# Performance work log

Measured on AMD Instinct MI355X. Metric: run time of the kernel, lower is better.

## Reference

```python
import jax, jax.numpy as jnp
import numpy as np

D_MODEL = 768
N_HEAD = 12
D_K = D_MODEL // N_HEAD  # 64, also d_v
B, S = 2, 2048


def setup_inputs() -> dict:
    key = jax.random.key(0)
    ks = jax.random.split(key, 8)
    scale = 1.0 / np.sqrt(D_MODEL)
    return {
        "q": jax.random.normal(ks[0], (B, S, D_MODEL), dtype=jnp.float32),
        "k": jax.random.normal(ks[1], (B, S, D_MODEL), dtype=jnp.float32),
        "v": jax.random.normal(ks[2], (B, S, D_MODEL), dtype=jnp.float32),
        "mask": jax.random.randint(ks[3], (B, 1, S, S), 0, 2, dtype=jnp.int32),
        # per-head projection weights, stacked over heads: [H, d_model, d_k]
        "Wq": jax.random.normal(ks[4], (N_HEAD, D_MODEL, D_K), dtype=jnp.float32) * scale,
        "Wk": jax.random.normal(ks[5], (N_HEAD, D_MODEL, D_K), dtype=jnp.float32) * scale,
        "Wv": jax.random.normal(ks[6], (N_HEAD, D_MODEL, D_K), dtype=jnp.float32) * scale,
        # output projection: [n_head*d_v, d_model]
        "Wo": jax.random.normal(ks[7], (N_HEAD * D_K, D_MODEL), dtype=jnp.float32) * scale,
    }


def reference(q, k, v, mask, Wq, Wk, Wv, Wo):
    # Per-head projections (batched over heads instead of a python loop)
    qh = jnp.einsum("bsd,hdk->bhsk", q, Wq)  # [B,H,S,d_k]
    kh = jnp.einsum("bsd,hdk->bhsk", k, Wk)
    vh = jnp.einsum("bsd,hdk->bhsk", v, Wv)
    # Scaled dot-product attention with full score matrix (faithful to source)
    scores = jnp.einsum("bhsk,bhtk->bhst", qh, kh) / jnp.sqrt(jnp.asarray(D_K, qh.dtype))
    scores = jnp.where(mask == 0, jnp.asarray(-1e9, scores.dtype), scores)
    attn = jax.nn.softmax(scores, axis=-1)  # [B,H,S,S]
    out = jnp.einsum("bhst,bhtk->bhsk", attn, vh)  # [B,H,S,d_k]
    # concat heads (matches torch.cat over head outputs along last dim)
    out = out.transpose(0, 2, 1, 3).reshape(out.shape[0], out.shape[2], -1)  # [B,S,H*d_k]
    return out @ Wo  # [B,S,d_model]
```

## Files before the change

kernel.cpp:

```cpp
#include <hip/hip_runtime.h>
#include <stdint.h>

#define S_LEN 2048
#define NH 12
#define DM 768
#define DK 64
#define NB 2
#define MROWS (NB * S_LEN)

typedef __attribute__((ext_vector_type(8))) short short8;
typedef __attribute__((ext_vector_type(4))) float f32x4;
typedef __attribute__((ext_vector_type(4))) uint32_t u32x4;

__device__ __forceinline__ unsigned short bf16rne(float f) {
    union { float f; uint32_t u; } v; v.f = f;
    return (unsigned short)((v.u + 0x7FFFu + ((v.u >> 16) & 1u)) >> 16);
}

__device__ __forceinline__ uint32_t cvtpk(float lo, float hi) {
    uint32_t r;
    asm("v_cvt_pk_bf16_f32 %0, %1, %2" : "=v"(r) : "v"(lo), "v"(hi));
    return r;
}

__global__ __launch_bounds__(256) void prep_kernel(
        const float* __restrict__ Wq, const float* __restrict__ Wk,
        const float* __restrict__ Wv, const float* __restrict__ Wo,
        const int* __restrict__ mask,
        unsigned short* __restrict__ WqT, unsigned short* __restrict__ WkT,
        unsigned short* __restrict__ WvT, unsigned short* __restrict__ WoT,
        uint32_t* __restrict__ pm) {
    int bx = blockIdx.x;
    if (bx < 9216) {
        int which = bx / 2304;
        const float* W = (which == 0) ? Wq : (which == 1) ? Wk : (which == 2) ? Wv : Wo;
        unsigned short* WT = (which == 0) ? WqT : (which == 1) ? WkT : (which == 2) ? WvT : WoT;
        int idx = (bx % 2304) * 256 + threadIdx.x;
        int n = idx / DM, kd = idx % DM;
        float val;
        if (which < 3) { int h = n >> 6, kk = n & 63; val = W[(h * DM + kd) * DK + kk]; }
        else          { val = W[kd * DM + n]; }
        if (which == 0) val *= 0.18033688011112042f;
        WT[idx] = bf16rne(val);
    } else {
        int t = (bx - 9216) * 256 + threadIdx.x;
        const int4* mp = (const int4*)mask;
        int4 a = mp[2 * t], b = mp[2 * t + 1];
        unsigned int by =
            (a.x != 0 ? 1u : 0u)  | (a.y != 0 ? 2u : 0u)  | (a.z != 0 ? 4u : 0u)  | (a.w != 0 ? 8u : 0u) |
            (b.x != 0 ? 16u : 0u) | (b.y != 0 ? 32u : 0u) | (b.z != 0 ? 64u : 0u) | (b.w != 0 ? 128u : 0u);
        ((unsigned char*)pm)[t] = (unsigned char)by;
    }
}

__device__ __forceinline__ void gemm_core_f32A(const float* __restrict__ A,
                                               const unsigned short* __restrict__ BT,
                                               unsigned short* As, unsigned short* Bs,
                                               f32x4 (&acc)[4][4]) {
    const int tid = threadIdx.x;
    const int lane = tid & 63, wid = tid >> 6;
    const int ww = wid & 1, wh = wid >> 1;
    const int quad = lane >> 4, l16 = lane & 15;
    const int lr = lane >> 2;
    const int lc = (lane & 3) * 8;
    typedef __attribute__((address_space(1))) const unsigned int* gp1;
    typedef __attribute__((address_space(3))) unsigned int* lp3;
    const float* Ag0 = A + (size_t)(wid * 32 + lr) * DM + lc;
    const float* Ag1 = A + (size_t)(wid * 32 + 16 + lr) * DM + lc;
    const unsigned short* Bg = BT + (size_t)(wid * 32 + lr) * DM + lc;
    unsigned short* Al = &As[wid * 32 * 32];
    unsigned short* Bl = &Bs[wid * 32 * 32];
    for (int kt = 0; kt < DM; kt += 32) {
        __syncthreads();
        __builtin_amdgcn_global_load_lds((gp1)(const void*)(Bg + kt),            (lp3)(void*)Bl,             16, 0, 0);
        __builtin_amdgcn_global_load_lds((gp1)(const void*)(Bg + 16 * DM + kt),  (lp3)(void*)(Bl + 16 * 32), 16, 0, 0);
        float4 x0 = *(const float4*)(Ag0 + kt), x1 = *(const float4*)(Ag0 + kt + 4);
        float4 y0 = *(const float4*)(Ag1 + kt), y1 = *(const float4*)(Ag1 + kt + 4);
        u32x4 ua, ub;
        ua[0] = cvtpk(x0.x, x0.y); ua[1] = cvtpk(x0.z, x0.w);
        ua[2] = cvtpk(x1.x, x1.y); ua[3] = cvtpk(x1.z, x1.w);
        ub[0] = cvtpk(y0.x, y0.y); ub[1] = cvtpk(y0.z, y0.w);
        ub[2] = cvtpk(y1.x, y1.y); ub[3] = cvtpk(y1.z, y1.w);
        *(u32x4*)&Al[lr * 32 + lc] = ua;
        *(u32x4*)&Al[(16 + lr) * 32 + lc] = ub;
        __syncthreads();
        short8 af[4], bf[4];
#pragma unroll
        for (int i = 0; i < 4; ++i) af[i] = *(const short8*)&As[(wh * 64 + i * 16 + l16) * 32 + quad * 8];
#pragma unroll
        for (int j = 0; j < 4; ++j) bf[j] = *(const short8*)&Bs[(ww * 64 + j * 16 + l16) * 32 + quad * 8];
#pragma unroll
        for (int i = 0; i < 4; ++i)
#pragma unroll
            for (int j = 0; j < 4; ++j)
                acc[i][j] = __builtin_amdgcn_mfma_f32_16x16x32_bf16(af[i], bf[j], acc[i][j], 0, 0, 0);
    }
}

__global__ __launch_bounds__(256) void proj_gemm(
        const float* __restrict__ qf32, const float* __restrict__ kf32,
        const float* __restrict__ vf32,
        const unsigned short* __restrict__ WqT, const unsigned short* __restrict__ WkT,
        const unsigned short* __restrict__ WvT,
        unsigned short* __restrict__ qh, unsigned short* __restrict__ kh,
        unsigned short* __restrict__ vhT) {
    __shared__ __align__(16) unsigned short As[128 * 32];
    __shared__ __align__(16) unsigned short Bs[128 * 32];
    const int z = blockIdx.z;
    const float* A = (z == 0) ? qf32 : (z == 1) ? kf32 : vf32;
    const unsigned short* BT = (z == 0) ? WqT : (z == 1) ? WkT : WvT;
    f32x4 acc[4][4] = {};
    gemm_core_f32A(A + (size_t)blockIdx.x * 128 * DM, BT + (size_t)blockIdx.y * 128 * DM, As, Bs, acc);

    const int tid = threadIdx.x;
    const int lane = tid & 63, wid = tid >> 6;
    const int ww = wid & 1, wh = wid >> 1;
    const int quad = lane >> 4, l16 = lane & 15;
    const int row0 = blockIdx.x * 128 + wh * 64;
    const int col0 = blockIdx.y * 128 + ww * 64;
    if (z < 2) {
        unsigned short* C = z ? kh : qh;
#pragma unroll
        for (int i = 0; i < 4; ++i)
#pragma unroll
            for (int j = 0; j < 4; ++j)
#pragma unroll
                for (int r = 0; r < 4; ++r)
                    C[(size_t)(row0 + i * 16 + quad * 4 + r) * DM + col0 + j * 16 + l16] = bf16rne(acc[i][j][r]);
    } else {
#pragma unroll
        for (int i = 0; i < 4; ++i)
#pragma unroll
            for (int j = 0; j < 4; ++j) {
                int row = row0 + i * 16 + quad * 4;
                int col = col0 + j * 16 + l16;
                int bb = row >> 11, s = row & 2047;
                int hh = col >> 6, d = col & 63;
                int g = (s >> 2) & 15;
                int pg = (g & 8) | ((g & 3) << 1) | ((g & 4) >> 2);
                int sp = (s & ~63) | (pg << 2) | (s & 3);
                uint32_t lo = (uint32_t)bf16rne(acc[i][j][0]) | ((uint32_t)bf16rne(acc[i][j][1]) << 16);
                uint32_t hi = (uint32_t)bf16rne(acc[i][j][2]) | ((uint32_t)bf16rne(acc[i][j][3]) << 16);
                uint2 o = make_uint2(lo, hi);
                *(uint2*)&vhT[(size_t)((bb * NH + hh) * DK + d) * S_LEN + sp] = o;
            }
    }
}

__global__ __launch_bounds__(256) void attn_kernel(
        const unsigned short* __restrict__ qh, const unsigned short* __restrict__ kh,
        const unsigned short* __restrict__ vhT, const uint32_t* __restrict__ pm,
        unsigned short* __restrict__ pob, float* __restrict__ lsb) {
    const int bid = blockIdx.x;
    const int xcd = bid & 7, pos = bid >> 3;
    const int wkr = xcd * 192 + pos;
    const int qt = wkr & 15;
    const int hz = wkr >> 4;
    const int h = hz % 12;
    const int z = hz / 12;
    const int b = z >> 2, ks = z & 3;
    const int tid = threadIdx.x, w = tid >> 6, lane = tid & 63;
    const int quad = lane >> 4, l16 = lane & 15;
    __shared__ __align__(16) unsigned short SMEM[2 * 64 * 64];
    unsigned short* Ks = SMEM;
    unsigned short* Vs = SMEM + 64 * 64;

    const int qrow0 = qt * 128 + w * 32;
    short8 qf[2][2];
#pragma unroll
    for (int mi = 0; mi < 2; ++mi) {
        const size_t qbase = (size_t)(b * S_LEN + qrow0 + mi * 16 + l16) * DM + h * DK;
        qf[mi][0] = *(const short8*)&qh[qbase + quad * 8];
        qf[mi][1] = *(const short8*)&qh[qbase + 32 + quad * 8];
    }
    short8 of = {};
    if (l16 == 0) {
#pragma unroll
        for (int j = 0; j < 8; ++j) of[j] = (short)0x3F80;
    }

    f32x4 out_t[2][4] = {};
    f32x4 outl[2] = {};

    const int srow = tid >> 2, scol = (tid & 3) << 4;
    const int ssw = (srow & 7) << 3;
    const int sc0 = srow * 64 + (scol ^ ssw);
    const int sc1 = srow * 64 + ((scol + 8) ^ ssw);
    const unsigned short* Kg = kh + (size_t)b * S_LEN * DM + h * DK;
    const unsigned short* Vg = vhT + (size_t)((b * NH + h) * DK) * S_LEN;
    const int kt0 = ks * (S_LEN / 4);

    short8 kr0, kr1, vr0, vr1;
    kr0 = *(const short8*)&Kg[(size_t)(kt0 + srow) * DM + scol];
    kr1 = *(const short8*)&Kg[(size_t)(kt0 + srow) * DM + scol + 8];
    vr0 = *(const short8*)&Vg[(size_t)srow * S_LEN + kt0 + scol];
    vr1 = *(const short8*)&Vg[(size_t)srow * S_LEN + kt0 + scol + 8];

    for (int kt = kt0; kt < kt0 + S_LEN / 4; kt += 64) {
        __syncthreads();
        *(short8*)&Ks[sc0] = kr0;
        *(short8*)&Ks[sc1] = kr1;
        *(short8*)&Vs[sc0] = vr0;
        *(short8*)&Vs[sc1] = vr1;
        __syncthreads();
        {
            const int kn = kt + 64;
            kr0 = *(const short8*)&Kg[(size_t)(kn + srow) * DM + scol];
            kr1 = *(const short8*)&Kg[(size_t)(kn + srow) * DM + scol + 8];
            vr0 = *(const short8*)&Vg[(size_t)srow * S_LEN + kn + scol];
            vr1 = *(const short8*)&Vg[(size_t)srow * S_LEN + kn + scol + 8];
        }
        uint2 mw[2];
#pragma unroll
        for (int mi = 0; mi < 2; ++mi)
            mw[mi] = *(const uint2*)&pm[(size_t)(b * S_LEN + qrow0 + mi * 16 + l16) * 64 + (kt >> 5)];

        u32x4 pf32[2][2];
#pragma unroll
        for (int cb = 0; cb < 4; ++cb) {
            const int krw = cb * 16 + l16, ksw = (krw & 7) << 3;
            short8 kf0 = *(const short8*)&Ks[krw * 64 + ((quad * 8) ^ ksw)];
            short8 kf1 = *(const short8*)&Ks[krw * 64 + ((32 + quad * 8) ^ ksw)];
#pragma unroll
            for (int mi = 0; mi < 2; ++mi) {
                f32x4 zz = {0.f, 0.f, 0.f, 0.f};
                zz = __builtin_amdgcn_mfma_f32_16x16x32_bf16(kf0, qf[mi][0], zz, 0, 0, 0);
                zz = __builtin_amdgcn_mfma_f32_16x16x32_bf16(kf1, qf[mi][1], zz, 0, 0, 0);
                uint32_t mword = (cb & 2) ? mw[mi].y : mw[mi].x;
                float e[4];
#pragma unroll
                for (int r = 0; r < 4; ++r) {
                    float ev = __builtin_amdgcn_exp2f(zz[r]);
                    int32_t mneg = __builtin_amdgcn_sbfe((int32_t)mword, ((cb & 1) << 4) + quad * 4 + r, 1);
                    e[r] = __uint_as_float(__float_as_uint(ev) & (uint32_t)mneg);
                }
                pf32[mi][cb >> 1][(cb & 1) * 2 + 0] = cvtpk(e[0], e[1]);
                pf32[mi][cb >> 1][(cb & 1) * 2 + 1] = cvtpk(e[2], e[3]);
            }
        }
        short8 pf[2][2];
#pragma unroll
        for (int mi = 0; mi < 2; ++mi) {
            pf[mi][0] = __builtin_bit_cast(short8, pf32[mi][0]);
            pf[mi][1] = __builtin_bit_cast(short8, pf32[mi][1]);
        }

        __builtin_amdgcn_s_setprio(1);
#pragma unroll
        for (int c2 = 0; c2 < 4; ++c2) {
            const int vrw = c2 * 16 + l16, vsw = (vrw & 7) << 3;
            short8 vf0 = *(const short8*)&Vs[vrw * 64 + ((quad * 8) ^ vsw)];
            short8 vf1 = *(const short8*)&Vs[vrw * 64 + ((32 + quad * 8) ^ vsw)];
#pragma unroll
            for (int mi = 0; mi < 2; ++mi) {
                out_t[mi][c2] = __builtin_amdgcn_mfma_f32_16x16x32_bf16(vf0, pf[mi][0], out_t[mi][c2], 0, 0, 0);
                out_t[mi][c2] = __builtin_amdgcn_mfma_f32_16x16x32_bf16(vf1, pf[mi][1], out_t[mi][c2], 0, 0, 0);
            }
        }
#pragma unroll
        for (int mi = 0; mi < 2; ++mi) {
            outl[mi] = __builtin_amdgcn_mfma_f32_16x16x32_bf16(of, pf[mi][0], outl[mi], 0, 0, 0);
            outl[mi] = __builtin_amdgcn_mfma_f32_16x16x32_bf16(of, pf[mi][1], outl[mi], 0, 0, 0);
        }
        __builtin_amdgcn_s_setprio(0);
    }

    const int pz = z;
    if (quad == 0) {
#pragma unroll
        for (int mi = 0; mi < 2; ++mi)
            lsb[((size_t)pz * NH + h) * S_LEN + qrow0 + mi * 16 + l16] = outl[mi][0];
    }

    __syncthreads();
    unsigned short* Os = SMEM + w * 2048;
#pragma unroll
    for (int mi = 0; mi < 2; ++mi) {
        const int orow = mi * 16 + l16, osw = (orow & 7) << 3;
#pragma unroll
        for (int c2 = 0; c2 < 4; ++c2) {
            uint2 pw2;
            pw2.x = cvtpk(out_t[mi][c2][0], out_t[mi][c2][1]);
            pw2.y = cvtpk(out_t[mi][c2][2], out_t[mi][c2][3]);
            *(uint2*)&Os[orow * 64 + ((c2 * 16 + quad * 4) ^ osw)] = pw2;
        }
    }
    const int ql = lane >> 1, hf = lane & 1;
    const int qsw = (ql & 7) << 3;
    const int qg = qrow0 + ql;
    const size_t orowg = ((size_t)pz * S_LEN + qg) * DM + h * DK + hf * 32;
#pragma unroll
    for (int k2 = 0; k2 < 4; ++k2)
        *(short8*)&pob[orowg + k2 * 8] = *(const short8*)&Os[ql * 64 + ((hf * 32 + k2 * 8) ^ qsw)];
}

__global__ __launch_bounds__(256) void out_gemm(
        const unsigned short* __restrict__ pob, const float* __restrict__ lsb,
        const unsigned short* __restrict__ WoT, float* __restrict__ C) {
    __shared__ __align__(16) unsigned short As[128 * 32];
    __shared__ __align__(16) unsigned short Bs[128 * 32];
    const int tid = threadIdx.x;
    const int lane = tid & 63, wid = tid >> 6;
    const int ww = wid & 1, wh = wid >> 1;
    const int quad = lane >> 4, l16 = lane & 15;
    const int lr = lane >> 2, lc = (lane & 3) * 8;
    typedef __attribute__((address_space(1))) const unsigned int* gp1;
    typedef __attribute__((address_space(3))) unsigned int* lp3;
    const int ra0 = blockIdx.x * 128 + wid * 32 + lr;
    const int ra1 = ra0 + 16;
    const int bb = blockIdx.x >> 4;
    const unsigned short* Bg = WoT + (size_t)(blockIdx.y * 128 + wid * 32 + lr) * DM + lc;
    unsigned short* Al = &As[wid * 32 * 32];
    unsigned short* Bl = &Bs[wid * 32 * 32];
    size_t oa0[4], oa1[4];
    int ol0[4], ol1[4];
#pragma unroll
    for (int ksp = 0; ksp < 4; ++ksp) {
        int pz = bb * 4 + ksp;
        oa0[ksp] = ((size_t)pz * S_LEN + (ra0 & 2047)) * DM + lc;
        oa1[ksp] = ((size_t)pz * S_LEN + (ra1 & 2047)) * DM + lc;
        ol0[ksp] = (pz * NH) * S_LEN + (ra0 & 2047);
        ol1[ksp] = (pz * NH) * S_LEN + (ra1 & 2047);
    }
    f32x4 acc[4][4] = {};
    for (int kt = 0; kt < DM; kt += 32) {
        __syncthreads();
        __builtin_amdgcn_global_load_lds((gp1)(const void*)(Bg + kt),           (lp3)(void*)Bl,            16, 0, 0);
        __builtin_amdgcn_global_load_lds((gp1)(const void*)(Bg + 16 * DM + kt), (lp3)(void*)(Bl + 16 * 32), 16, 0, 0);
        const int hh = kt >> 6;
        float l0 = 0.f, l1 = 0.f;
        short8 p0[4], p1[4];
#pragma unroll
        for (int ksp = 0; ksp < 4; ++ksp) {
            p0[ksp] = *(const short8*)&pob[oa0[ksp] + kt];
            p1[ksp] = *(const short8*)&pob[oa1[ksp] + kt];
            l0 += lsb[ol0[ksp] + hh * S_LEN];
            l1 += lsb[ol1[ksp] + hh * S_LEN];
        }
        float rl0 = 1.f / fmaxf(l0, 1e-37f);
        float rl1 = 1.f / fmaxf(l1, 1e-37f);
        u32x4 ua, ub;
#pragma unroll
        for (int e = 0; e < 4; ++e) {
            float f0lo = 0.f, f0hi = 0.f, f1lo = 0.f, f1hi = 0.f;
#pragma unroll
            for (int ksp = 0; ksp < 4; ++ksp) {
                uint32_t w0 = ((const u32x4&)p0[ksp])[e];
                uint32_t w1 = ((const u32x4&)p1[ksp])[e];
                f0lo += __uint_as_float(w0 << 16);
                f0hi += __uint_as_float(w0 & 0xFFFF0000u);
                f1lo += __uint_as_float(w1 << 16);
                f1hi += __uint_as_float(w1 & 0xFFFF0000u);
            }
            ua[e] = cvtpk(f0lo * rl0, f0hi * rl0);
            ub[e] = cvtpk(f1lo * rl1, f1hi * rl1);
        }
        *(u32x4*)&Al[lr * 32 + lc] = ua;
        *(u32x4*)&Al[(16 + lr) * 32 + lc] = ub;
        __syncthreads();
        short8 af[4], bf[4];
#pragma unroll
        for (int i = 0; i < 4; ++i) af[i] = *(const short8*)&As[(wh * 64 + i * 16 + l16) * 32 + quad * 8];
#pragma unroll
        for (int j = 0; j < 4; ++j) bf[j] = *(const short8*)&Bs[(ww * 64 + j * 16 + l16) * 32 + quad * 8];
#pragma unroll
        for (int i = 0; i < 4; ++i)
#pragma unroll
            for (int j = 0; j < 4; ++j)
                acc[i][j] = __builtin_amdgcn_mfma_f32_16x16x32_bf16(af[i], bf[j], acc[i][j], 0, 0, 0);
    }
    const int row0 = blockIdx.x * 128 + wh * 64;
    const int col0 = blockIdx.y * 128 + ww * 64;
#pragma unroll
    for (int i = 0; i < 4; ++i)
#pragma unroll
        for (int j = 0; j < 4; ++j)
#pragma unroll
            for (int r = 0; r < 4; ++r)
                C[(size_t)(row0 + i * 16 + quad * 4 + r) * DM + col0 + j * 16 + l16] = acc[i][j][r];
}

extern "C" void kernel_launch(void* const* d_in, const int* in_sizes, int n_in,
                              void* d_out, int out_size, void* d_ws, size_t ws_size,
                              hipStream_t stream) {
    const float* q = (const float*)d_in[0];
    const float* k = (const float*)d_in[1];
    const float* v = (const float*)d_in[2];
    const int* mask = (const int*)d_in[3];
    const float* Wq = (const float*)d_in[4];
    const float* Wk = (const float*)d_in[5];
    const float* Wv = (const float*)d_in[6];
    const float* Wo = (const float*)d_in[7];
    float* out = (float*)d_out;

    char* ws = (char*)d_ws;
    size_t off = 0;
    auto alloc = [&](size_t bytes) {
        void* p = ws + off;
        off += (bytes + 255) & ~(size_t)255;
        return p;
    };
    const size_t MAT = (size_t)MROWS * DM * 2;
    const size_t WMAT = (size_t)DM * DM * 2;
    unsigned short* WoT = (unsigned short*)alloc(WMAT);
    unsigned short* qh  = (unsigned short*)alloc(MAT);
    unsigned short* kh  = (unsigned short*)alloc(MAT);
    unsigned short* vhT = (unsigned short*)alloc(MAT);
    uint32_t* pmask     = (uint32_t*)alloc((size_t)NB * S_LEN * 64 * 4);
    float* lsb          = (float*)alloc((size_t)8 * NH * S_LEN * 4);
    unsigned short* WqT = (unsigned short*)alloc(WMAT);
    unsigned short* WkT = (unsigned short*)alloc(WMAT);
    unsigned short* WvT = (unsigned short*)alloc(WMAT);
    unsigned short* pob = WqT;
    (void)alloc((size_t)8 * S_LEN * DM * 2 - 3 * WMAT);

    prep_kernel<<<dim3(9216 + 4096), 256, 0, stream>>>(Wq, Wk, Wv, Wo, mask,
                                                       WqT, WkT, WvT, WoT, pmask);
    proj_gemm<<<dim3(32, 6, 3), 256, 0, stream>>>(q, k, v, WqT, WkT, WvT, qh, kh, vhT);
    attn_kernel<<<dim3(1536), 256, 0, stream>>>(qh, kh, vhT, pmask, pob, lsb);
    out_gemm<<<dim3(32, 6), 256, 0, stream>>>(pob, lsb, WoT, out);
}
```

Baseline: 239.4 us.

## Double-buffer K/V tiles in attention and remap GEMM blocks per XCD

The attention kernel now keeps two shared-memory K/V buffers. The next tile is written into the idle buffer after compute, which removes one of the two barriers per iteration. The projection and output GEMMs switch to a 1D grid whose block index is remapped so neighbouring tiles land on the same XCD, aiming for better L2 reuse of shared A/B panels. The cost is doubled LDS use in attention (32KB), which may reduce occupancy.

```diff
diff --git a/kernel.cpp b/kernel.cpp
--- a/kernel.cpp
+++ b/kernel.cpp
@@ -106,18 +106,22 @@
         unsigned short* __restrict__ vhT) {
     __shared__ __align__(16) unsigned short As[128 * 32];
     __shared__ __align__(16) unsigned short Bs[128 * 32];
-    const int z = blockIdx.z;
+    const int bid = blockIdx.x;
+    const int xcd = bid & 7, pos = bid >> 3;
+    const int widx = xcd * 72 + pos;
+    const int oi = widx / 6, by = widx % 6;
+    const int z = oi >> 5, bx = oi & 31;
     const float* A = (z == 0) ? qf32 : (z == 1) ? kf32 : vf32;
     const unsigned short* BT = (z == 0) ? WqT : (z == 1) ? WkT : WvT;
     f32x4 acc[4][4] = {};
-    gemm_core_f32A(A + (size_t)blockIdx.x * 128 * DM, BT + (size_t)blockIdx.y * 128 * DM, As, Bs, acc);
+    gemm_core_f32A(A + (size_t)bx * 128 * DM, BT + (size_t)by * 128 * DM, As, Bs, acc);
 
     const int tid = threadIdx.x;
     const int lane = tid & 63, wid = tid >> 6;
     const int ww = wid & 1, wh = wid >> 1;
     const int quad = lane >> 4, l16 = lane & 15;
-    const int row0 = blockIdx.x * 128 + wh * 64;
-    const int col0 = blockIdx.y * 128 + ww * 64;
+    const int row0 = bx * 128 + wh * 64;
+    const int col0 = by * 128 + ww * 64;
     if (z < 2) {
         unsigned short* C = z ? kh : qh;
 #pragma unroll
@@ -161,9 +165,7 @@
     const int b = z >> 2, ks = z & 3;
     const int tid = threadIdx.x, w = tid >> 6, lane = tid & 63;
     const int quad = lane >> 4, l16 = lane & 15;
-    __shared__ __align__(16) unsigned short SMEM[2 * 64 * 64];
-    unsigned short* Ks = SMEM;
-    unsigned short* Vs = SMEM + 64 * 64;
+    __shared__ __align__(16) unsigned short SMEM[2 * 2 * 64 * 64];
 
     const int qrow0 = qt * 128 + w * 32;
     short8 qf[2][2];
@@ -189,21 +191,26 @@
     const unsigned short* Kg = kh + (size_t)b * S_LEN * DM + h * DK;
     const unsigned short* Vg = vhT + (size_t)((b * NH + h) * DK) * S_LEN;
     const int kt0 = ks * (S_LEN / 4);
-
-    short8 kr0, kr1, vr0, vr1;
-    kr0 = *(const short8*)&Kg[(size_t)(kt0 + srow) * DM + scol];
-    kr1 = *(const short8*)&Kg[(size_t)(kt0 + srow) * DM + scol + 8];
-    vr0 = *(const short8*)&Vg[(size_t)srow * S_LEN + kt0 + scol];
-    vr1 = *(const short8*)&Vg[(size_t)srow * S_LEN + kt0 + scol + 8];
-
-    for (int kt = kt0; kt < kt0 + S_LEN / 4; kt += 64) {
-        __syncthreads();
-        *(short8*)&Ks[sc0] = kr0;
-        *(short8*)&Ks[sc1] = kr1;
-        *(short8*)&Vs[sc0] = vr0;
-        *(short8*)&Vs[sc1] = vr1;
-        __syncthreads();
-        {
+    const int NT = (S_LEN / 4) / 64;
+
+    {
+        short8 a0 = *(const short8*)&Kg[(size_t)(kt0 + srow) * DM + scol];
+        short8 a1 = *(const short8*)&Kg[(size_t)(kt0 + srow) * DM + scol + 8];
+        short8 a2 = *(const short8*)&Vg[(size_t)srow * S_LEN + kt0 + scol];
+        short8 a3 = *(const short8*)&Vg[(size_t)srow * S_LEN + kt0 + scol + 8];
+        *(short8*)&SMEM[sc0] = a0;
+        *(short8*)&SMEM[sc1] = a1;
+        *(short8*)&SMEM[4096 + sc0] = a2;
+        *(short8*)&SMEM[4096 + sc1] = a3;
+    }
+    __syncthreads();
+
+    int cur = 0;
+    for (int t = 0; t < NT; ++t) {
+        const int kt = kt0 + t * 64;
+        const bool more = (t + 1 < NT);
+        short8 kr0, kr1, vr0, vr1;
+        if (more) {
             const int kn = kt + 64;
             kr0 = *(const short8*)&Kg[(size_t)(kn + srow) * DM + scol];
             kr1 = *(const short8*)&Kg[(size_t)(kn + srow) * DM + scol + 8];
@@ -214,6 +221,9 @@
 #pragma unroll
         for (int mi = 0; mi < 2; ++mi)
             mw[mi] = *(const uint2*)&pm[(size_t)(b * S_LEN + qrow0 + mi * 16 + l16) * 64 + (kt >> 5)];
+
+        const unsigned short* Ks = SMEM + cur * 8192;
+        const unsigned short* Vs = Ks + 4096;
 
         u32x4 pf32[2][2];
 #pragma unroll
@@ -263,6 +273,16 @@
             outl[mi] = __builtin_amdgcn_mfma_f32_16x16x32_bf16(of, pf[mi][1], outl[mi], 0, 0, 0);
         }
         __builtin_amdgcn_s_setprio(0);
+
+        if (more) {
+            unsigned short* Kn = SMEM + (cur ^ 1) * 8192;
+            *(short8*)&Kn[sc0] = kr0;
+            *(short8*)&Kn[sc1] = kr1;
+            *(short8*)&Kn[4096 + sc0] = vr0;
+            *(short8*)&Kn[4096 + sc1] = vr1;
+            __syncthreads();
+            cur ^= 1;
+        }
     }
 
     const int pz = z;
@@ -299,6 +319,10 @@
         const unsigned short* __restrict__ WoT, float* __restrict__ C) {
     __shared__ __align__(16) unsigned short As[128 * 32];
     __shared__ __align__(16) unsigned short Bs[128 * 32];
+    const int bid = blockIdx.x;
+    const int xcd = bid & 7, pos = bid >> 3;
+    const int widx = xcd * 24 + pos;
+    const int bx = widx / 6, by = widx % 6;
     const int tid = threadIdx.x;
     const int lane = tid & 63, wid = tid >> 6;
     const int ww = wid & 1, wh = wid >> 1;
@@ -306,10 +330,10 @@
     const int lr = lane >> 2, lc = (lane & 3) * 8;
     typedef __attribute__((address_space(1))) const unsigned int* gp1;
     typedef __attribute__((address_space(3))) unsigned int* lp3;
-    const int ra0 = blockIdx.x * 128 + wid * 32 + lr;
+    const int ra0 = bx * 128 + wid * 32 + lr;
     const int ra1 = ra0 + 16;
-    const int bb = blockIdx.x >> 4;
-    const unsigned short* Bg = WoT + (size_t)(blockIdx.y * 128 + wid * 32 + lr) * DM + lc;
+    const int bb = bx >> 4;
+    const unsigned short* Bg = WoT + (size_t)(by * 128 + wid * 32 + lr) * DM + lc;
     unsigned short* Al = &As[wid * 32 * 32];
     unsigned short* Bl = &Bs[wid * 32 * 32];
     size_t oa0[4], oa1[4];
@@ -369,8 +393,8 @@
             for (int j = 0; j < 4; ++j)
                 acc[i][j] = __builtin_amdgcn_mfma_f32_16x16x32_bf16(af[i], bf[j], acc[i][j], 0, 0, 0);
     }
-    const int row0 = blockIdx.x * 128 + wh * 64;
-    const int col0 = blockIdx.y * 128 + ww * 64;
+    const int row0 = bx * 128 + wh * 64;
+    const int col0 = by * 128 + ww * 64;
 #pragma unroll
     for (int i = 0; i < 4; ++i)
 #pragma unroll
@@ -416,7 +440,7 @@
 
     prep_kernel<<<dim3(9216 + 4096), 256, 0, stream>>>(Wq, Wk, Wv, Wo, mask,
                                                        WqT, WkT, WvT, WoT, pmask);
-    proj_gemm<<<dim3(32, 6, 3), 256, 0, stream>>>(q, k, v, WqT, WkT, WvT, qh, kh, vhT);
+    proj_gemm<<<dim3(576), 256, 0, stream>>>(q, k, v, WqT, WkT, WvT, qh, kh, vhT);
     attn_kernel<<<dim3(1536), 256, 0, stream>>>(qh, kh, vhT, pmask, pob, lsb);
-    out_gemm<<<dim3(32, 6), 256, 0, stream>>>(pob, lsb, WoT, out);
-}
+    out_gemm<<<dim3(192), 256, 0, stream>>>(pob, lsb, WoT, out);
+}
```

New measurement: 239.7 us. No clear change (+0.1%).
